# Kernel tuning notes

Hardware: AMD Instinct MI355X
Metric: run time of the kernel (lower is better)

Reference implementation:

```python
import jax, jax.numpy as jnp
import numpy as np

N_NODES = 100000
N_EDGES = 1600000
NODE_IN = 64
EDGE_DIM = 32
NODE_OUT = 64


def setup_inputs() -> dict:
    key = jax.random.key(0)
    ks = jax.random.split(key, 8)
    return {
        "nfeats": jax.random.normal(ks[0], (N_NODES, NODE_IN), dtype=jnp.float32),
        "efeats": jax.random.normal(ks[1], (N_EDGES, EDGE_DIM), dtype=jnp.float32),
        "src": jax.random.randint(ks[2], (N_EDGES,), 0, N_NODES, dtype=jnp.int32),
        "dst": jax.random.randint(ks[3], (N_EDGES,), 0, N_NODES, dtype=jnp.int32),
        "W_msg_w": jax.random.normal(ks[4], (NODE_IN + EDGE_DIM, NODE_OUT), dtype=jnp.float32) * 0.1,
        "W_msg_b": jax.random.normal(ks[5], (NODE_OUT,), dtype=jnp.float32) * 0.1,
        "W_apply_w": jax.random.normal(ks[6], (NODE_IN + NODE_OUT, NODE_OUT), dtype=jnp.float32) * 0.1,
        "W_apply_b": jax.random.normal(ks[7], (NODE_OUT,), dtype=jnp.float32) * 0.1,
    }


def reference(nfeats, efeats, src, dst, W_msg_w, W_msg_b, W_apply_w, W_apply_b):
    n_nodes = nfeats.shape[0]
    # message: gather source node features, concat edge features, linear
    m = jnp.concatenate([nfeats[src], efeats], axis=-1) @ W_msg_w + W_msg_b  # [E, node_out]
    # per-destination mean (DGL fn.mean); zero for isolated nodes
    s = jax.ops.segment_sum(m, dst, num_segments=n_nodes)                     # [N, node_out]
    cnt = jax.ops.segment_sum(jnp.ones((m.shape[0],), m.dtype), dst, num_segments=n_nodes)
    h_neigh = s / jnp.maximum(cnt, 1.0)[:, None]
    # apply: concat self features with aggregated messages, linear, activation
    h = jnp.concatenate([nfeats, h_neigh], axis=-1) @ W_apply_w + W_apply_b   # [N, node_out]
    return jax.nn.relu(h)
```

## Files before the change

### kernel.cpp

```cpp
#include <hip/hip_runtime.h>

#define NN 100000
#define NE 1600000
#define NBIN 782
#define CAP  3072
#define EPB  8192
#define NBLKE 196

#define OFF_RS      0
#define OFF_BINSZ   100004
#define OFF_BINBASE 100788
#define OFF_MASK    101572
#define OFF_EINFO   300520
#define OFF_G       3500520
#define OFF_HM      OFF_G
#define OFF_OM      (OFF_G + 153272)
#define OFF_WCOMB   13100520
#define OFF_BMW     13110760

__global__ __launch_bounds__(256) void k_bhist(const int4* __restrict__ dst4,
                                               int* __restrict__ hm) {
  __shared__ int h[NBIN];
  int b = blockIdx.x, t = threadIdx.x;
  for (int i = t; i < NBIN; i += 256) h[i] = 0;
  __syncthreads();
  int e0 = b * EPB;
#pragma unroll
  for (int i = 0; i < EPB / 1024; ++i) {
    int f = i * 256 + t;
    int e = e0 + f * 4;
    if (e < NE) {
      int4 d = dst4[(e0 >> 2) + f];
      atomicAdd(&h[d.x >> 7], 1);
      atomicAdd(&h[d.y >> 7], 1);
      atomicAdd(&h[d.z >> 7], 1);
      atomicAdd(&h[d.w >> 7], 1);
    }
  }
  __syncthreads();
  for (int i = t; i < NBIN; i += 256) hm[b * NBIN + i] = h[i];
}

__global__ __launch_bounds__(256) void k_bscan(const int* __restrict__ hm,
                                               int* __restrict__ om,
                                               int* __restrict__ binsz) {
  int w = (blockIdx.x * 256 + threadIdx.x) >> 6;
  int lane = threadIdx.x & 63;
  if (w >= NBIN) return;
  int carry = 0;
  for (int base = 0; base < NBLKE; base += 64) {
    int b = base + lane;
    int v = (b < NBLKE) ? hm[b * NBIN + w] : 0;
    int inc = v;
#pragma unroll
    for (int off = 1; off < 64; off <<= 1) {
      int x = __shfl_up(inc, off);
      if (lane >= off) inc += x;
    }
    if (b < NBLKE) om[b * NBIN + w] = carry + inc - v;
    carry += __shfl(inc, 63);
  }
  if (lane == 0) binsz[w] = carry;
}

__global__ __launch_bounds__(1024) void k_binscan(const int* __restrict__ binsz,
                                                  int* __restrict__ binbase) {
  __shared__ int s[1024];
  int t = threadIdx.x;
  int v = (t < NBIN) ? binsz[t] : 0;
  s[t] = v; __syncthreads();
#pragma unroll
  for (int off = 1; off < 1024; off <<= 1) {
    int x = (t >= off) ? s[t - off] : 0;
    __syncthreads();
    s[t] += x;
    __syncthreads();
  }
  if (t <= NBIN) binbase[t] = s[t] - v;
}

__global__ __launch_bounds__(256) void k_bplace(
    const int4* __restrict__ src4, const int4* __restrict__ dst4,
    const int* __restrict__ om, const int* __restrict__ binbase,
    int2* __restrict__ einfo) {
  __shared__ int2 buf[EPB];
  __shared__ int hstart[1024];
  __shared__ int hcur[1024];
  __shared__ int obase[NBIN];
  __shared__ int tscan[256];
  int b = blockIdx.x, t = threadIdx.x;
  int e0 = b * EPB;
  for (int i = t; i < 1024; i += 256) hcur[i] = 0;
  for (int i = t; i < NBIN; i += 256) obase[i] = binbase[i] + om[b * NBIN + i];
  __syncthreads();
#pragma unroll
  for (int i = 0; i < EPB / 1024; ++i) {
    int f = i * 256 + t;
    int e = e0 + f * 4;
    if (e < NE) {
      int4 d = dst4[(e0 >> 2) + f];
      atomicAdd(&hcur[d.x >> 7], 1);
      atomicAdd(&hcur[d.y >> 7], 1);
      atomicAdd(&hcur[d.z >> 7], 1);
      atomicAdd(&hcur[d.w >> 7], 1);
    }
  }
  __syncthreads();
  int base4 = t * 4;
  int v0 = hcur[base4], v1 = hcur[base4 + 1], v2 = hcur[base4 + 2], v3 = hcur[base4 + 3];
  int s = v0 + v1 + v2 + v3;
  tscan[t] = s;
  __syncthreads();
#pragma unroll
  for (int off = 1; off < 256; off <<= 1) {
    int x = (t >= off) ? tscan[t - off] : 0;
    __syncthreads();
    tscan[t] += x;
    __syncthreads();
  }
  int texcl = tscan[t] - s;
  hstart[base4]     = texcl;
  hstart[base4 + 1] = texcl + v0;
  hstart[base4 + 2] = texcl + v0 + v1;
  hstart[base4 + 3] = texcl + v0 + v1 + v2;
  __syncthreads();
  for (int i = t; i < 1024; i += 256) hcur[i] = hstart[i];
  __syncthreads();
#pragma unroll
  for (int i = 0; i < EPB / 1024; ++i) {
    int f = i * 256 + t;
    int e = e0 + f * 4;
    if (e < NE) {
      int4 d = dst4[(e0 >> 2) + f];
      int4 sv = src4[(e0 >> 2) + f];
      int p0 = atomicAdd(&hcur[d.x >> 7], 1);
      int p1 = atomicAdd(&hcur[d.y >> 7], 1);
      int p2 = atomicAdd(&hcur[d.z >> 7], 1);
      int p3 = atomicAdd(&hcur[d.w >> 7], 1);
      buf[p0] = make_int2(sv.x | ((d.x & 127) << 20), (e)     | ((d.x >> 7) << 21));
      buf[p1] = make_int2(sv.y | ((d.y & 127) << 20), (e + 1) | ((d.y >> 7) << 21));
      buf[p2] = make_int2(sv.z | ((d.z & 127) << 20), (e + 2) | ((d.z >> 7) << 21));
      buf[p3] = make_int2(sv.w | ((d.w & 127) << 20), (e + 3) | ((d.w >> 7) << 21));
    }
  }
  __syncthreads();
  int nE = NE - e0; if (nE > EPB) nE = EPB;
  for (int i = t; i < nE; i += 256) {
    int2 r = buf[i];
    int bin = (unsigned)r.y >> 21;
    int pos = obase[bin] + (i - hstart[bin]);
    einfo[pos] = make_int2(r.x, r.y & 0x1FFFFF);
  }
}

__global__ __launch_bounds__(256) void k_sortbin(const int* __restrict__ binbase,
                                                 int* __restrict__ rs,
                                                 float* __restrict__ mask,
                                                 int2* __restrict__ einfo) {
  __shared__ int hist[128];
  __shared__ int excl[128];
  __shared__ int2 buf[CAP];
  int b = blockIdx.x, t = threadIdx.x;
  int base = binbase[b];
  int nE = binbase[b + 1] - base;
  int nS = nE < CAP ? nE : CAP;
  if (t < 128) hist[t] = 0;
  __syncthreads();
  for (int i = t; i < nS; i += 256) {
    int2 v = einfo[base + i];
    buf[i] = v;
    atomicAdd(&hist[(v.x >> 20) & 127], 1);
  }
  __syncthreads();
  int myc = 0;
  if (t < 128) { myc = hist[t]; excl[t] = myc; }
  __syncthreads();
#pragma unroll
  for (int off = 1; off < 128; off <<= 1) {
    int x = 0;
    if (t < 128 && t >= off) x = excl[t - off];
    __syncthreads();
    if (t < 128) excl[t] += x;
    __syncthreads();
  }
  if (t < 128) {
    int node = b * 128 + t;
    if (node < NN) {
      rs[node] = base + excl[t] - myc;
      mask[node] = myc ? 1.f : 0.f;
    }
    hist[t] = t ? excl[t - 1] : 0;
  }
  if (b == NBIN - 1 && t == 0) rs[NN] = NE;
  __syncthreads();
  for (int i = t; i < nS; i += 256) {
    int2 v = buf[i];
    int dl = (v.x >> 20) & 127;
    int p = atomicAdd(&hist[dl], 1);
    einfo[base + p] = make_int2(v.x & 0xFFFFF, v.y);
  }
  for (int i = nS + t; i < nE; i += 256)
    atomicAnd((int*)&einfo[base + i].x, 0xFFFFF);
}

__global__ __launch_bounds__(256) void k_gather(
    const float* __restrict__ nf, const float* __restrict__ ef,
    const int2* __restrict__ einfo, const int* __restrict__ rs,
    float* __restrict__ g) {
  int wid = threadIdx.x >> 6, lane = threadIdx.x & 63;
  int n0 = (blockIdx.x * 4 + wid) * 4;
  int r = (lane < 5) ? rs[n0 + lane] : 0;
  int beg = __builtin_amdgcn_readlane(r, 0);
  int end = __builtin_amdgcn_readlane(r, 4);
  bool hi = lane >= 32;
  int l32 = lane & 31;
  float a0 = 0.f, a1 = 0.f;
  int curk = 0;
  int cbeg = beg;
  int nxt = __builtin_amdgcn_readlane(r, 1);
  for (int base = beg; base < end; base += 64) {
    int nb = end - base; if (nb > 64) nb = 64;
    int2 info = (lane < nb) ? einfo[base + lane] : make_int2(0, 0);
    int off = 0;
    while (off < nb) {
      int stop = nxt - base; if (stop > nb) stop = nb;
      int j = off;
      for (; j + 8 <= stop; j += 8) {
        int s0 = __builtin_amdgcn_readlane(info.x, j);
        int s1 = __builtin_amdgcn_readlane(info.x, j + 1);
        int s2 = __builtin_amdgcn_readlane(info.x, j + 2);
        int s3 = __builtin_amdgcn_readlane(info.x, j + 3);
        int s4 = __builtin_amdgcn_readlane(info.x, j + 4);
        int s5 = __builtin_amdgcn_readlane(info.x, j + 5);
        int s6 = __builtin_amdgcn_readlane(info.x, j + 6);
        int s7 = __builtin_amdgcn_readlane(info.x, j + 7);
        int ep0 = hi ? __builtin_amdgcn_readlane(info.y, j + 1)
                     : __builtin_amdgcn_readlane(info.y, j);
        int ep1 = hi ? __builtin_amdgcn_readlane(info.y, j + 3)
                     : __builtin_amdgcn_readlane(info.y, j + 2);
        int ep2 = hi ? __builtin_amdgcn_readlane(info.y, j + 5)
                     : __builtin_amdgcn_readlane(info.y, j + 4);
        int ep3 = hi ? __builtin_amdgcn_readlane(info.y, j + 7)
                     : __builtin_amdgcn_readlane(info.y, j + 6);
        float v0 = nf[s0 * 64 + lane];
        float v1 = nf[s1 * 64 + lane];
        float v2 = nf[s2 * 64 + lane];
        float v3 = nf[s3 * 64 + lane];
        float v4 = nf[s4 * 64 + lane];
        float v5 = nf[s5 * 64 + lane];
        float v6 = nf[s6 * 64 + lane];
        float v7 = nf[s7 * 64 + lane];
        float w0 = ef[ep0 * 32 + l32];
        float w1 = ef[ep1 * 32 + l32];
        float w2 = ef[ep2 * 32 + l32];
        float w3 = ef[ep3 * 32 + l32];
        a0 += ((v0 + v1) + (v2 + v3)) + ((v4 + v5) + (v6 + v7));
        a1 += (w0 + w1) + (w2 + w3);
      }
      for (; j + 2 <= stop; j += 2) {
        int s0 = __builtin_amdgcn_readlane(info.x, j);
        int s1 = __builtin_amdgcn_readlane(info.x, j + 1);
        int ep = hi ? __builtin_amdgcn_readlane(info.y, j + 1)
                    : __builtin_amdgcn_readlane(info.y, j);
        float v0 = nf[s0 * 64 + lane];
        float v1 = nf[s1 * 64 + lane];
        float w0 = ef[ep * 32 + l32];
        a0 += v0 + v1;
        a1 += w0;
      }
      if (j < stop) {
        int s0 = __builtin_amdgcn_readlane(info.x, j);
        int e0 = __builtin_amdgcn_readlane(info.y, j);
        a0 += nf[s0 * 64 + lane];
        if (!hi) a1 += ef[e0 * 32 + l32];
      }
      off = stop;
      if (nxt - base <= nb) {
        float a1f = a1 + __shfl_down(a1, 32);
        int node = n0 + curk;
        int degk = nxt - cbeg;
        float inv = degk > 0 ? 1.f / (float)degk : 0.f;
        g[node * 96 + lane] = a0 * inv;
        if (!hi) g[node * 96 + 64 + l32] = a1f * inv;
        a0 = 0.f; a1 = 0.f;
        ++curk;
        cbeg = nxt;
        if (curk < 4) nxt = __builtin_amdgcn_readlane(r, curk + 1);
        else break;
      }
    }
    if (curk >= 4) break;
  }
  while (curk < 4) {
    int node = n0 + curk;
    g[node * 96 + lane] = 0.f;
    if (!hi) g[node * 96 + 64 + l32] = 0.f;
    ++curk;
  }
}

__global__ __launch_bounds__(256) void k_pre1(
    const float* __restrict__ Wm, const float* __restrict__ bm,
    const float* __restrict__ Wa, float* __restrict__ Wcomb,
    float* __restrict__ bmW) {
  int b = blockIdx.x, t = threadIdx.x;
  if (b < 24) {
    int o = b * 256 + t;
    int k = o >> 6, j = o & 63;
    float acc = 0.f;
    for (int kk = 0; kk < 64; ++kk)
      acc += Wm[k * 64 + kk] * Wa[(64 + kk) * 64 + j];
    Wcomb[(64 + k) * 64 + j] = acc;
  } else {
    for (int i = t; i < 64 * 64; i += 256) Wcomb[i] = Wa[i];
    if (t < 64) {
      float acc = 0.f;
      for (int kk = 0; kk < 64; ++kk) acc += bm[kk] * Wa[(64 + kk) * 64 + t];
      bmW[t] = acc;
    }
  }
}

__global__ __launch_bounds__(256) void k_main(
    const float4* __restrict__ nf4, const float4* __restrict__ g4,
    const float* __restrict__ mask,
    const float4* __restrict__ Wcomb4, const float* __restrict__ bmW,
    const float* __restrict__ ba, float* __restrict__ out) {
  __shared__ float sA[128 * 33];
  __shared__ float sB[32 * 64];
  int tid = threadIdx.x;
  int ty = tid >> 3, tx = tid & 7;
  int nbase = blockIdx.x * 128;
  float acc[4][8];
#pragma unroll
  for (int r = 0; r < 4; ++r)
#pragma unroll
    for (int e = 0; e < 8; ++e) acc[r][e] = 0.f;

  for (int c = 0; c < 5; ++c) {
#pragma unroll
    for (int i = 0; i < 4; ++i) {
      int f = i * 256 + tid;
      int nl = f >> 3, q = f & 7;
      int node = nbase + nl; if (node > NN - 1) node = NN - 1;
      float4 v;
      if (c < 2) {
        v = nf4[node * 16 + c * 8 + q];
      } else {
        v = g4[node * 24 + (c - 2) * 8 + q];
      }
      float* p = &sA[nl * 33 + q * 4];
      p[0] = v.x; p[1] = v.y; p[2] = v.z; p[3] = v.w;
    }
#pragma unroll
    for (int i = 0; i < 2; ++i) {
      int f = i * 256 + tid;
      int kk = f >> 4, j4 = f & 15;
      float4 w = Wcomb4[(c * 32 + kk) * 16 + j4];
      *(float4*)&sB[kk * 64 + j4 * 4] = w;
    }
    __syncthreads();
#pragma unroll 8
    for (int kk = 0; kk < 32; ++kk) {
      float4 b0 = *(const float4*)&sB[kk * 64 + tx * 8];
      float4 b1 = *(const float4*)&sB[kk * 64 + tx * 8 + 4];
#pragma unroll
      for (int r = 0; r < 4; ++r) {
        float a = sA[(ty * 4 + r) * 33 + kk];
        acc[r][0] += a * b0.x; acc[r][1] += a * b0.y;
        acc[r][2] += a * b0.z; acc[r][3] += a * b0.w;
        acc[r][4] += a * b1.x; acc[r][5] += a * b1.y;
        acc[r][6] += a * b1.z; acc[r][7] += a * b1.w;
      }
    }
    __syncthreads();
  }
  float4 ba0 = ((const float4*)ba)[tx * 2];
  float4 ba1 = ((const float4*)ba)[tx * 2 + 1];
  float4 bw0 = ((const float4*)bmW)[tx * 2];
  float4 bw1 = ((const float4*)bmW)[tx * 2 + 1];
#pragma unroll
  for (int r = 0; r < 4; ++r) {
    int node = nbase + ty * 4 + r;
    if (node < NN) {
      float mk = mask[node];
      float4 o0, o1;
      o0.x = acc[r][0] + ba0.x + mk * bw0.x;
      o0.y = acc[r][1] + ba0.y + mk * bw0.y;
      o0.z = acc[r][2] + ba0.z + mk * bw0.z;
      o0.w = acc[r][3] + ba0.w + mk * bw0.w;
      o1.x = acc[r][4] + ba1.x + mk * bw1.x;
      o1.y = acc[r][5] + ba1.y + mk * bw1.y;
      o1.z = acc[r][6] + ba1.z + mk * bw1.z;
      o1.w = acc[r][7] + ba1.w + mk * bw1.w;
      o0.x = fmaxf(o0.x, 0.f); o0.y = fmaxf(o0.y, 0.f);
      o0.z = fmaxf(o0.z, 0.f); o0.w = fmaxf(o0.w, 0.f);
      o1.x = fmaxf(o1.x, 0.f); o1.y = fmaxf(o1.y, 0.f);
      o1.z = fmaxf(o1.z, 0.f); o1.w = fmaxf(o1.w, 0.f);
      *(float4*)&out[node * 64 + tx * 8] = o0;
      *(float4*)&out[node * 64 + tx * 8 + 4] = o1;
    }
  }
}

extern "C" void kernel_launch(void* const* d_in, const int* in_sizes, int n_in,
                              void* d_out, int out_size, void* d_ws, size_t ws_size,
                              hipStream_t stream) {
  const float* nf = (const float*)d_in[0];
  const float* ef = (const float*)d_in[1];
  const int*   src = (const int*)d_in[2];
  const int*   dst = (const int*)d_in[3];
  const float* Wm = (const float*)d_in[4];
  const float* bm = (const float*)d_in[5];
  const float* Wa = (const float*)d_in[6];
  const float* ba = (const float*)d_in[7];
  int*   wsi = (int*)d_ws;
  float* wsf = (float*)d_ws;
  int*   rs      = wsi + OFF_RS;
  int*   binsz   = wsi + OFF_BINSZ;
  int*   binbase = wsi + OFF_BINBASE;
  int2*  einfo   = (int2*)(wsi + OFF_EINFO);
  int*   hm      = wsi + OFF_HM;
  int*   om      = wsi + OFF_OM;
  float* mask    = wsf + OFF_MASK;
  float* g       = wsf + OFF_G;
  float* Wcomb   = wsf + OFF_WCOMB;
  float* bmW     = wsf + OFF_BMW;
  float* out = (float*)d_out;

  k_pre1<<<25, 256, 0, stream>>>(Wm, bm, Wa, Wcomb, bmW);
  k_bhist<<<NBLKE, 256, 0, stream>>>((const int4*)dst, hm);
  k_bscan<<<(NBIN * 64 + 255) / 256, 256, 0, stream>>>(hm, om, binsz);
  k_binscan<<<1, 1024, 0, stream>>>(binsz, binbase);
  k_bplace<<<NBLKE, 256, 0, stream>>>((const int4*)src, (const int4*)dst, om,
                                      binbase, einfo);
  k_sortbin<<<NBIN, 256, 0, stream>>>(binbase, rs, mask, einfo);
  k_gather<<<NN / 16, 256, 0, stream>>>(nf, ef, einfo, rs, g);
  k_main<<<(NN + 127) / 128, 256, 0, stream>>>(
      (const float4*)nf, (const float4*)g, mask,
      (const float4*)Wcomb, bmW, ba, out);
}
```

Baseline: 185.6 us.

## Fuse per-bin sort and neighbor gather into one kernel using LDS-resident edges

Merges the bin sort and gather kernels into a single kernel. Each block sorts its bin's edges by destination in shared memory and then gathers source-node and edge features directly from that LDS buffer. The goal is to drop the global writeback and re-read of the sorted edge list, the row-start array and one kernel launch. In exchange the gather runs with far fewer, larger blocks (one per bin, eight waves each), which lowers parallelism for a latency-bound gather. Edges beyond the LDS capacity of a bin are no longer handled.

```diff
diff --git a/kernel.cpp b/kernel.cpp
--- a/kernel.cpp
+++ b/kernel.cpp
@@ -7,7 +7,6 @@
 #define EPB  8192
 #define NBLKE 196
 
-#define OFF_RS      0
 #define OFF_BINSZ   100004
 #define OFF_BINBASE 100788
 #define OFF_MASK    101572
@@ -153,23 +152,30 @@
   }
 }
 
-__global__ __launch_bounds__(256) void k_sortbin(const int* __restrict__ binbase,
-                                                 int* __restrict__ rs,
-                                                 float* __restrict__ mask,
-                                                 int2* __restrict__ einfo) {
+__global__ __launch_bounds__(512, 6) void k_sortgather(
+    const float* __restrict__ nf, const float* __restrict__ ef,
+    const int2* __restrict__ einfo, const int* __restrict__ binbase,
+    float* __restrict__ g, float* __restrict__ mask) {
+  __shared__ int2 buf[CAP];
   __shared__ int hist[128];
   __shared__ int excl[128];
-  __shared__ int2 buf[CAP];
+  __shared__ int sstart[129];
   int b = blockIdx.x, t = threadIdx.x;
   int base = binbase[b];
   int nE = binbase[b + 1] - base;
   int nS = nE < CAP ? nE : CAP;
   if (t < 128) hist[t] = 0;
   __syncthreads();
-  for (int i = t; i < nS; i += 256) {
-    int2 v = einfo[base + i];
-    buf[i] = v;
-    atomicAdd(&hist[(v.x >> 20) & 127], 1);
+  int2 myreg[6];
+#pragma unroll
+  for (int i = 0; i < 6; ++i) {
+    int idx = i * 512 + t;
+    if (idx < nS) {
+      myreg[i] = einfo[base + idx];
+      atomicAdd(&hist[(myreg[i].x >> 20) & 127], 1);
+    } else {
+      myreg[i] = make_int2(-1, 0);
+    }
   }
   __syncthreads();
   int myc = 0;
@@ -185,117 +191,79 @@
   }
   if (t < 128) {
     int node = b * 128 + t;
-    if (node < NN) {
-      rs[node] = base + excl[t] - myc;
-      mask[node] = myc ? 1.f : 0.f;
-    }
-    hist[t] = t ? excl[t - 1] : 0;
-  }
-  if (b == NBIN - 1 && t == 0) rs[NN] = NE;
-  __syncthreads();
-  for (int i = t; i < nS; i += 256) {
-    int2 v = buf[i];
-    int dl = (v.x >> 20) & 127;
-    int p = atomicAdd(&hist[dl], 1);
-    einfo[base + p] = make_int2(v.x & 0xFFFFF, v.y);
-  }
-  for (int i = nS + t; i < nE; i += 256)
-    atomicAnd((int*)&einfo[base + i].x, 0xFFFFF);
-}
-
-__global__ __launch_bounds__(256) void k_gather(
-    const float* __restrict__ nf, const float* __restrict__ ef,
-    const int2* __restrict__ einfo, const int* __restrict__ rs,
-    float* __restrict__ g) {
-  int wid = threadIdx.x >> 6, lane = threadIdx.x & 63;
-  int n0 = (blockIdx.x * 4 + wid) * 4;
-  int r = (lane < 5) ? rs[n0 + lane] : 0;
-  int beg = __builtin_amdgcn_readlane(r, 0);
-  int end = __builtin_amdgcn_readlane(r, 4);
+    if (node < NN) mask[node] = myc ? 1.f : 0.f;
+    sstart[t] = excl[t] - myc;
+    hist[t] = excl[t] - myc;
+    if (t == 127) sstart[128] = excl[127];
+  }
+  __syncthreads();
+#pragma unroll
+  for (int i = 0; i < 6; ++i) {
+    if (myreg[i].x >= 0) {
+      int dl = (myreg[i].x >> 20) & 127;
+      int p = atomicAdd(&hist[dl], 1);
+      buf[p] = make_int2(myreg[i].x & 0xFFFFF, myreg[i].y);
+    }
+  }
+  __syncthreads();
+  int wv = t >> 6, lane = t & 63;
   bool hi = lane >= 32;
   int l32 = lane & 31;
-  float a0 = 0.f, a1 = 0.f;
-  int curk = 0;
-  int cbeg = beg;
-  int nxt = __builtin_amdgcn_readlane(r, 1);
-  for (int base = beg; base < end; base += 64) {
-    int nb = end - base; if (nb > 64) nb = 64;
-    int2 info = (lane < nb) ? einfo[base + lane] : make_int2(0, 0);
-    int off = 0;
-    while (off < nb) {
-      int stop = nxt - base; if (stop > nb) stop = nb;
-      int j = off;
-      for (; j + 8 <= stop; j += 8) {
-        int s0 = __builtin_amdgcn_readlane(info.x, j);
-        int s1 = __builtin_amdgcn_readlane(info.x, j + 1);
-        int s2 = __builtin_amdgcn_readlane(info.x, j + 2);
-        int s3 = __builtin_amdgcn_readlane(info.x, j + 3);
-        int s4 = __builtin_amdgcn_readlane(info.x, j + 4);
-        int s5 = __builtin_amdgcn_readlane(info.x, j + 5);
-        int s6 = __builtin_amdgcn_readlane(info.x, j + 6);
-        int s7 = __builtin_amdgcn_readlane(info.x, j + 7);
-        int ep0 = hi ? __builtin_amdgcn_readlane(info.y, j + 1)
-                     : __builtin_amdgcn_readlane(info.y, j);
-        int ep1 = hi ? __builtin_amdgcn_readlane(info.y, j + 3)
-                     : __builtin_amdgcn_readlane(info.y, j + 2);
-        int ep2 = hi ? __builtin_amdgcn_readlane(info.y, j + 5)
-                     : __builtin_amdgcn_readlane(info.y, j + 4);
-        int ep3 = hi ? __builtin_amdgcn_readlane(info.y, j + 7)
-                     : __builtin_amdgcn_readlane(info.y, j + 6);
-        float v0 = nf[s0 * 64 + lane];
-        float v1 = nf[s1 * 64 + lane];
-        float v2 = nf[s2 * 64 + lane];
-        float v3 = nf[s3 * 64 + lane];
-        float v4 = nf[s4 * 64 + lane];
-        float v5 = nf[s5 * 64 + lane];
-        float v6 = nf[s6 * 64 + lane];
-        float v7 = nf[s7 * 64 + lane];
-        float w0 = ef[ep0 * 32 + l32];
-        float w1 = ef[ep1 * 32 + l32];
-        float w2 = ef[ep2 * 32 + l32];
-        float w3 = ef[ep3 * 32 + l32];
-        a0 += ((v0 + v1) + (v2 + v3)) + ((v4 + v5) + (v6 + v7));
-        a1 += (w0 + w1) + (w2 + w3);
-      }
-      for (; j + 2 <= stop; j += 2) {
-        int s0 = __builtin_amdgcn_readlane(info.x, j);
-        int s1 = __builtin_amdgcn_readlane(info.x, j + 1);
-        int ep = hi ? __builtin_amdgcn_readlane(info.y, j + 1)
-                    : __builtin_amdgcn_readlane(info.y, j);
-        float v0 = nf[s0 * 64 + lane];
-        float v1 = nf[s1 * 64 + lane];
-        float w0 = ef[ep * 32 + l32];
-        a0 += v0 + v1;
-        a1 += w0;
-      }
-      if (j < stop) {
-        int s0 = __builtin_amdgcn_readlane(info.x, j);
-        int e0 = __builtin_amdgcn_readlane(info.y, j);
-        a0 += nf[s0 * 64 + lane];
-        if (!hi) a1 += ef[e0 * 32 + l32];
-      }
-      off = stop;
-      if (nxt - base <= nb) {
-        float a1f = a1 + __shfl_down(a1, 32);
-        int node = n0 + curk;
-        int degk = nxt - cbeg;
-        float inv = degk > 0 ? 1.f / (float)degk : 0.f;
-        g[node * 96 + lane] = a0 * inv;
-        if (!hi) g[node * 96 + 64 + l32] = a1f * inv;
-        a0 = 0.f; a1 = 0.f;
-        ++curk;
-        cbeg = nxt;
-        if (curk < 4) nxt = __builtin_amdgcn_readlane(r, curk + 1);
-        else break;
-      }
-    }
-    if (curk >= 4) break;
-  }
-  while (curk < 4) {
-    int node = n0 + curk;
-    g[node * 96 + lane] = 0.f;
-    if (!hi) g[node * 96 + 64 + l32] = 0.f;
-    ++curk;
+  for (int k = 0; k < 16; ++k) {
+    int dl = wv * 16 + k;
+    int node = b * 128 + dl;
+    if (node >= NN) break;
+    int beg = sstart[dl], end = sstart[dl + 1];
+    int deg = end - beg;
+    float a0 = 0.f, a1 = 0.f;
+    int j = beg;
+    for (; j + 8 <= end; j += 8) {
+      int2 q0 = buf[j + 0];
+      int2 q1 = buf[j + 1];
+      int2 q2 = buf[j + 2];
+      int2 q3 = buf[j + 3];
+      int2 q4 = buf[j + 4];
+      int2 q5 = buf[j + 5];
+      int2 q6 = buf[j + 6];
+      int2 q7 = buf[j + 7];
+      int ep0 = hi ? q1.y : q0.y;
+      int ep1 = hi ? q3.y : q2.y;
+      int ep2 = hi ? q5.y : q4.y;
+      int ep3 = hi ? q7.y : q6.y;
+      float v0 = nf[q0.x * 64 + lane];
+      float v1 = nf[q1.x * 64 + lane];
+      float v2 = nf[q2.x * 64 + lane];
+      float v3 = nf[q3.x * 64 + lane];
+      float v4 = nf[q4.x * 64 + lane];
+      float v5 = nf[q5.x * 64 + lane];
+      float v6 = nf[q6.x * 64 + lane];
+      float v7 = nf[q7.x * 64 + lane];
+      float w0 = ef[ep0 * 32 + l32];
+      float w1 = ef[ep1 * 32 + l32];
+      float w2 = ef[ep2 * 32 + l32];
+      float w3 = ef[ep3 * 32 + l32];
+      a0 += ((v0 + v1) + (v2 + v3)) + ((v4 + v5) + (v6 + v7));
+      a1 += (w0 + w1) + (w2 + w3);
+    }
+    for (; j + 2 <= end; j += 2) {
+      int2 q0 = buf[j];
+      int2 q1 = buf[j + 1];
+      int ep = hi ? q1.y : q0.y;
+      float v0 = nf[q0.x * 64 + lane];
+      float v1 = nf[q1.x * 64 + lane];
+      float w0 = ef[ep * 32 + l32];
+      a0 += v0 + v1;
+      a1 += w0;
+    }
+    if (j < end) {
+      int2 q0 = buf[j];
+      a0 += nf[q0.x * 64 + lane];
+      if (!hi) a1 += ef[q0.y * 32 + l32];
+    }
+    a1 += __shfl_down(a1, 32);
+    float inv = deg > 0 ? 1.f / (float)deg : 0.f;
+    g[node * 96 + lane] = a0 * inv;
+    if (!hi) g[node * 96 + 64 + l32] = a1 * inv;
   }
 }
 
@@ -416,7 +384,6 @@
   const float* ba = (const float*)d_in[7];
   int*   wsi = (int*)d_ws;
   float* wsf = (float*)d_ws;
-  int*   rs      = wsi + OFF_RS;
   int*   binsz   = wsi + OFF_BINSZ;
   int*   binbase = wsi + OFF_BINBASE;
   int2*  einfo   = (int2*)(wsi + OFF_EINFO);
@@ -434,8 +401,7 @@
   k_binscan<<<1, 1024, 0, stream>>>(binsz, binbase);
   k_bplace<<<NBLKE, 256, 0, stream>>>((const int4*)src, (const int4*)dst, om,
                                       binbase, einfo);
-  k_sortbin<<<NBIN, 256, 0, stream>>>(binbase, rs, mask, einfo);
-  k_gather<<<NN / 16, 256, 0, stream>>>(nf, ef, einfo, rs, g);
+  k_sortgather<<<NBIN, 512, 0, stream>>>(nf, ef, einfo, binbase, g, mask);
   k_main<<<(NN + 127) / 128, 256, 0, stream>>>(
       (const float4*)nf, (const float4*)g, mask,
       (const float4*)Wcomb, bmW, ba, out);
```

Result: no change. 184.5 us (-0.6%).
